# Kernel tuning notes

Hardware: AMD Instinct MI355X
Metric: run time of the kernel (lower is better)

The kernel has to match this reference:

```python
import jax, jax.numpy as jnp
import numpy as np

DIM = 768
HEADS = 12
HEAD_DIM = DIM // HEADS
NUM_CLASSES = 1000
SCALE = HEAD_DIM ** (-0.5)


def setup_inputs() -> dict:
    key = jax.random.key(0)
    ks = jax.random.split(key, 6)
    B, N = 4, 2048
    s = 0.02
    return {
        "x": jax.random.normal(ks[0], (B, N, DIM), dtype=jnp.float32),
        "w_qkv": jax.random.normal(ks[1], (DIM, 3 * DIM), dtype=jnp.float32) * s,
        "w_proj": jax.random.normal(ks[2], (DIM, DIM), dtype=jnp.float32) * s,
        "b_proj": jax.random.normal(ks[3], (DIM,), dtype=jnp.float32) * s,
        "w_head": jax.random.normal(ks[4], (DIM, NUM_CLASSES), dtype=jnp.float32) * s,
        "b_head": jax.random.normal(ks[5], (NUM_CLASSES,), dtype=jnp.float32) * s,
    }


def reference(x, w_qkv, w_proj, b_proj, w_head, b_head):
    B, N, C = x.shape
    qkv = (x @ w_qkv).reshape(B, N, 3, HEADS, HEAD_DIM)
    qkv = jnp.transpose(qkv, (2, 0, 3, 1, 4))  # [3, B, H, N, hd]
    q, k, v = qkv[0], qkv[1], qkv[2]
    attn = jnp.einsum("bhnd,bhmd->bhnm", q, k) * SCALE  # [B,H,N,N]
    attn = jax.nn.softmax(attn, axis=-1)
    out = jnp.einsum("bhnm,bhmd->bhnd", attn, v)  # [B,H,N,hd]
    out = jnp.transpose(out, (0, 2, 1, 3)).reshape(B, N, C)
    out = out @ w_proj + b_proj
    out = out @ w_head + b_head  # [B,N,num_classes]
    return jnp.max(out, axis=1)  # [B,num_classes]
```

## Files before the change

### kernel.cpp

```cpp
#include <hip/hip_runtime.h>
#include <hip/hip_bf16.h>

typedef __attribute__((ext_vector_type(8))) short short8;
typedef __attribute__((ext_vector_type(4))) float f32x4;
typedef __attribute__((ext_vector_type(16))) float f32x16;
typedef unsigned short u16t;
typedef unsigned int u32t;

#define MFMA16(a, b, c) __builtin_amdgcn_mfma_f32_16x16x32_bf16((a), (b), (c), 0, 0, 0)
#define MFMA32(a, b, c) __builtin_amdgcn_mfma_f32_32x32x16_bf16((a), (b), (c), 0, 0, 0)

__device__ __forceinline__ u16t f2b(float f) {
    union { float f; u32t u; } v; v.f = f;
    u32t u = v.u + 0x7FFFu + ((v.u >> 16) & 1u);
    return (u16t)(u >> 16);
}
__device__ __forceinline__ u32t encf(float f) {
    union { float f; u32t u; } v; v.f = f;
    return (v.u & 0x80000000u) ? ~v.u : (v.u | 0x80000000u);
}
__device__ __forceinline__ float decf(u32t u) {
    union { u32t u; float f; } v;
    v.u = (u & 0x80000000u) ? (u ^ 0x80000000u) : ~u;
    return v.f;
}
__device__ __forceinline__ float fexp2(float x) {
#if __has_builtin(__builtin_amdgcn_exp2f)
    return __builtin_amdgcn_exp2f(x);
#else
    return __expf(x * 0.6931471805599453f);
#endif
}
__device__ __forceinline__ void gload16(const u16t* g, u16t* l) {
    __builtin_amdgcn_global_load_lds((const __attribute__((address_space(1))) void*)g,
                                     (__attribute__((address_space(3))) void*)l, 16, 0, 0);
}

__global__ __launch_bounds__(256) void k_cast_x(const float* __restrict__ x, u16t* __restrict__ xb) {
    int i = blockIdx.x * 256 + threadIdx.x;
    float4 v = ((const float4*)x)[i];
    ushort4 o;
    o.x = f2b(v.x); o.y = f2b(v.y); o.z = f2b(v.z); o.w = f2b(v.w);
    ((ushort4*)xb)[i] = o;
}

__global__ __launch_bounds__(256) void k_transpose(const float* __restrict__ W, u16t* __restrict__ WT,
                                                   int K, int N, int NP) {
    __shared__ float t[32][33];
    int n0 = blockIdx.x * 32, k0 = blockIdx.y * 32;
    int tx = threadIdx.x, ty = threadIdx.y;
    for (int i = 0; i < 32; i += 8) {
        int k = k0 + ty + i, n = n0 + tx;
        t[ty + i][tx] = (n < N) ? W[(size_t)k * N + n] : 0.f;
    }
    __syncthreads();
    for (int i = 0; i < 32; i += 8) {
        int n = n0 + ty + i, k = k0 + tx;
        if (n < NP) WT[(size_t)n * K + k] = f2b(t[tx][ty + i]);
    }
}

__global__ __launch_bounds__(256) void k_bias_f(const float* __restrict__ bproj, const float* __restrict__ whead,
                                                const float* __restrict__ bhead, float* __restrict__ bf) {
    __shared__ float red[256];
    int t = threadIdx.x;
    int c = t & 15;
    int jg = t >> 4;
    int n = blockIdx.x * 16 + c;
    float s = 0.f;
    if (n < 1000) {
#pragma unroll 4
        for (int j = jg * 48; j < jg * 48 + 48; ++j)
            s += bproj[j] * whead[j * 1000 + n];
    }
    red[t] = s;
    __syncthreads();
    for (int off = 128; off >= 16; off >>= 1) {
        if (t < off) red[t] += red[t + off];
        __syncthreads();
    }
    if (t < 16) {
        int nn = blockIdx.x * 16 + t;
        bf[nn] = (nn < 1000) ? (red[t] + bhead[nn]) : 0.f;
    }
}

__global__ __launch_bounds__(256) void k_init_out(u32t* __restrict__ o, int n) {
    int i = blockIdx.x * 256 + threadIdx.x;
    if (i < n) o[i] = 0u;
}
__global__ __launch_bounds__(256) void k_decode_out(u32t* __restrict__ o, int n) {
    int i = blockIdx.x * 256 + threadIdx.x;
    if (i < n) {
        float f = decf(o[i]);
        ((float*)o)[i] = f;
    }
}

#define BM 256
#define BN 128

#define QSCALE 0.18033688011112042f

template <int EPI>
__global__ __launch_bounds__(512, 2) void k_gemm8(const u16t* __restrict__ A, const u16t* __restrict__ BT,
                                                  int M, int N, int K,
                                                  u16t* __restrict__ Cb, const float* __restrict__ bias,
                                                  u32t* __restrict__ omax) {
    __shared__ alignas(16) u16t Asf[2 * 2 * 8192];
    __shared__ alignas(16) u16t Bsf[2 * 2 * 4096];

    int tid = threadIdx.x;
    int lane = tid & 63, wid = tid >> 6;
    int wr = wid >> 1, wc = wid & 1;
    int g = lane >> 4, l15 = lane & 15;

    int nwg = gridDim.x;
    int bid = blockIdx.x;
    int wg = (bid & 7) * (nwg >> 3) + (bid >> 3);
    int nx = N >> 7;
    int bx = wg % nx, by = wg / nx;
    int m0 = by * BM, n0 = bx * BN;

    f32x4 acc[4][4];
    for (int i = 0; i < 4; i++)
        for (int j = 0; j < 4; j++) acc[i][j] = (f32x4){0.f, 0.f, 0.f, 0.f};

    const u16t* srcA[4]; u16t* dstA[4];
#pragma unroll
    for (int ii = 0; ii < 4; ii++) {
        int kk = ii >> 1;
        int cl = wid * 128 + (ii & 1) * 64 + lane;
        int cd = cl ^ ((cl >> 3) & 3);
        int arow = cd >> 2, acolc = cd & 3;
        srcA[ii] = A + (size_t)(m0 + arow) * K + kk * 32 + acolc * 8;
        dstA[ii] = &Asf[kk * 8192 + cl * 8];
    }
    const u16t* srcB[2]; u16t* dstB[2];
#pragma unroll
    for (int jj = 0; jj < 2; jj++) {
        int c = (wid * 2 + jj) * 64 + lane;
        int kk = c >> 9, cl = c & 511;
        int cd = cl ^ ((cl >> 3) & 3);
        srcB[jj] = BT + (size_t)(n0 + (cd >> 2)) * K + kk * 32 + (cd & 3) * 8;
        dstB[jj] = &Bsf[kk * 4096 + cl * 8];
    }

    int aoff[4], boff[4];
#pragma unroll
    for (int i = 0; i < 4; i++) {
        int lin = ((wr * 64 + i * 16 + l15) << 6) + (g << 4);
        aoff[i] = (lin ^ (((lin >> 7) & 3) << 4)) >> 1;
    }
#pragma unroll
    for (int j = 0; j < 4; j++) {
        int lin = ((wc * 64 + j * 16 + l15) << 6) + (g << 4);
        boff[j] = (lin ^ (((lin >> 7) & 3) << 4)) >> 1;
    }

#pragma unroll
    for (int ii = 0; ii < 4; ii++) gload16(srcA[ii], dstA[ii]);
#pragma unroll
    for (int jj = 0; jj < 2; jj++) gload16(srcB[jj], dstB[jj]);

    const int NT = K >> 6;

#pragma unroll 1
    for (int t = 0; t < NT; ++t) {
        const int d = t & 1, nd = d ^ 1;
        if (t + 1 < NT) {
            int ko = (t + 1) << 6;
            gload16(srcA[0] + ko, dstA[0] + nd * 16384);
            gload16(srcA[1] + ko, dstA[1] + nd * 16384);
            gload16(srcB[0] + ko, dstB[0] + nd * 8192);
            gload16(srcB[1] + ko, dstB[1] + nd * 8192);
            asm volatile("s_waitcnt vmcnt(4)" ::: "memory");
        } else {
            asm volatile("s_waitcnt vmcnt(0)" ::: "memory");
        }
        __builtin_amdgcn_s_barrier();

        const u16t* Ab = &Asf[d * 16384];
        const u16t* Bb = &Bsf[d * 8192];

        short8 af[4], bf[4];
#pragma unroll
        for (int i = 0; i < 4; i++) af[i] = *(const short8*)&Ab[aoff[i]];
#pragma unroll
        for (int j = 0; j < 4; j++) bf[j] = *(const short8*)&Bb[boff[j]];
        __builtin_amdgcn_s_setprio(1);
#pragma unroll
        for (int i = 0; i < 4; i++)
#pragma unroll
            for (int j = 0; j < 4; j++) acc[i][j] = MFMA16(af[i], bf[j], acc[i][j]);
        __builtin_amdgcn_s_setprio(0);

        if (t + 1 < NT) {
            int ko = (t + 1) << 6;
            gload16(srcA[2] + ko, dstA[2] + nd * 16384);
            gload16(srcA[3] + ko, dstA[3] + nd * 16384);
        }

#pragma unroll
        for (int i = 0; i < 4; i++) af[i] = *(const short8*)&Ab[8192 + aoff[i]];
#pragma unroll
        for (int j = 0; j < 4; j++) bf[j] = *(const short8*)&Bb[4096 + boff[j]];
        __builtin_amdgcn_s_setprio(1);
#pragma unroll
        for (int i = 0; i < 4; i++)
#pragma unroll
            for (int j = 0; j < 4; j++) acc[i][j] = MFMA16(af[i], bf[j], acc[i][j]);
        __builtin_amdgcn_s_setprio(0);

        asm volatile("s_waitcnt lgkmcnt(0)" ::: "memory");
        __builtin_amdgcn_s_barrier();
    }

    if constexpr (EPI == 0) {
        for (int i = 0; i < 4; i++)
            for (int j = 0; j < 4; j++)
                for (int r = 0; r < 4; r++) {
                    int row = m0 + wr * 64 + i * 16 + g * 4 + r;
                    int col = n0 + wc * 64 + j * 16 + l15;
                    int t = col / 768, rem = col - t * 768;
                    int hh = rem >> 6, d = rem & 63;
                    int bb = row >> 11, n = row & 2047;
                    float v = acc[i][j][r];
                    size_t idx;
                    if (t == 0) {
                        v *= QSCALE;
                        idx = ((size_t)(bb * 12 + hh)) * 131072 + (size_t)n * 64 + d;
                    } else if (t == 1) {
                        idx = ((size_t)(48 + bb * 12 + hh)) * 131072 + (size_t)n * 64 + d;
                    } else {
                        int np = (n & ~12) | ((n & 4) << 1) | ((n & 8) >> 1);
                        idx = ((size_t)(96 + bb * 12 + hh)) * 131072 + (size_t)d * 2048 + np;
                    }
                    Cb[idx] = f2b(v);
                }
    } else if constexpr (EPI == 3) {
        for (int i = 0; i < 4; i++)
            for (int j = 0; j < 4; j++)
                for (int r = 0; r < 4; r++) {
                    int row = m0 + wr * 64 + i * 16 + g * 4 + r;
                    int col = n0 + wc * 64 + j * 16 + l15;
                    Cb[(size_t)row * N + col] = f2b(acc[i][j][r]);
                }
    } else {
        __shared__ float smax[4][BN];
        float cmax[4];
        for (int j = 0; j < 4; j++) {
            float m = -3.0e38f;
            for (int i = 0; i < 4; i++)
                for (int r = 0; r < 4; r++) m = fmaxf(m, acc[i][j][r]);
            m = fmaxf(m, __shfl_xor(m, 16));
            m = fmaxf(m, __shfl_xor(m, 32));
            cmax[j] = m;
        }
        __syncthreads();
        if (lane < 16)
            for (int j = 0; j < 4; j++) smax[wr][wc * 64 + j * 16 + lane] = cmax[j];
        __syncthreads();
        if (tid < BN) {
            int col = n0 + tid;
            if (col < 1000) {
                float m = fmaxf(fmaxf(smax[0][tid], smax[1][tid]),
                                fmaxf(smax[2][tid], smax[3][tid])) + bias[col];
                int b = m0 >> 11;
                atomicMax(&omax[b * 1000 + col], encf(m));
            }
        }
    }
}

__global__ __launch_bounds__(256) void k_flash(const u16t* __restrict__ QKV, u16t* __restrict__ AO) {
    __shared__ alignas(16) u16t Kc[3][4096];
    __shared__ alignas(16) u16t Vc[3][4096];

    const int tid = threadIdx.x;
    const int lane = tid & 63;
    const int h = lane >> 5;
    const int l31 = lane & 31;
    const int w = tid >> 6;
    const int wk = ((blockIdx.x & 7) * 96) + (blockIdx.x >> 3);
    const int qt = wk & 15;
    const int hb = wk >> 4;
    const int head = hb % 12, b = hb / 12;
    const u16t* Qg = QKV + ((size_t)hb) * 131072;
    const u16t* Kg = QKV + ((size_t)(48 + hb)) * 131072;
    const u16t* Vg = QKV + ((size_t)(96 + hb)) * 131072;
    const int q0w = qt * 128 + w * 32;

    short8 qf[4];
#pragma unroll
    for (int ks = 0; ks < 4; ++ks)
        qf[ks] = *(const short8*)&Qg[(size_t)(q0w + l31) * 64 + ks * 16 + h * 8];
    asm volatile("s_waitcnt vmcnt(0)" ::: "memory");

    short8 vone;
#pragma unroll
    for (int e = 0; e < 8; ++e) vone[e] = (short)0x3F80;

    f32x16 o0, o1, lsum;
#pragma unroll
    for (int r = 0; r < 16; ++r) { o0[r] = 0.f; o1[r] = 0.f; lsum[r] = 0.f; }

    auto stage = [&](int bi, int kv0) {
#pragma unroll
        for (int c = 0; c < 2; ++c) {
            int ic = c * 256 + tid;
            int ss = ic >> 8, ks = (ic >> 6) & 3, l6 = ic & 63;
            int hh = l6 >> 5, lq = l6 & 31;
            const u16t* gs = Kg + ((size_t)(kv0 + ss * 32 + lq) << 6) + ks * 16 + hh * 8;
            gload16(gs, &Kc[bi][ic * 8]);
        }
#pragma unroll
        for (int c = 0; c < 2; ++c) {
            int ic = c * 256 + tid;
            int jb = ic >> 8, ks = (ic >> 6) & 3, l6 = ic & 63;
            int hh = l6 >> 5, ld = l6 & 31;
            const u16t* gs = Vg + (size_t)(jb * 32 + ld) * 2048 + kv0 + ks * 16 + hh * 8;
            gload16(gs, &Vc[bi][ic * 8]);
        }
    };

    stage(0, 0);
    stage(1, 64);

#pragma unroll 1
    for (int t = 0; t < 32; ++t) {
        const int cur = t % 3;
        if (t < 30) {
            stage((t + 2) % 3, (t + 2) * 64);
            asm volatile("s_waitcnt vmcnt(8)" ::: "memory");
        } else if (t == 30) {
            asm volatile("s_waitcnt vmcnt(4)" ::: "memory");
        } else {
            asm volatile("s_waitcnt vmcnt(0)" ::: "memory");
        }
        __builtin_amdgcn_s_barrier();

        const u16t* Kb = &Kc[cur][0];
        const u16t* Vb = &Vc[cur][0];

        f32x16 s0, s1;
#pragma unroll
        for (int r = 0; r < 16; ++r) { s0[r] = 0.f; s1[r] = 0.f; }
        __builtin_amdgcn_s_setprio(1);
#pragma unroll
        for (int ks = 0; ks < 4; ++ks) {
            short8 k0 = *(const short8*)&Kb[(ks * 64 + lane) * 8];
            short8 k1 = *(const short8*)&Kb[((4 + ks) * 64 + lane) * 8];
            s0 = MFMA32(k0, qf[ks], s0);
            s1 = MFMA32(k1, qf[ks], s1);
        }
        __builtin_amdgcn_s_setprio(0);

        short8 pf[4];
        auto packhalf = [&](const f32x16& sv, int half, int idx) {
            union { u32t wu[4]; short8 v; } u;
#pragma unroll
            for (int wq = 0; wq < 4; ++wq) {
                float lo = fexp2(sv[half * 8 + 2 * wq]);
                float hi = fexp2(sv[half * 8 + 2 * wq + 1]);
                asm("v_cvt_pk_bf16_f32 %0, %1, %2" : "=v"(u.wu[wq]) : "v"(lo), "v"(hi));
            }
            pf[idx] = u.v;
        };
        packhalf(s0, 0, 0);
        packhalf(s0, 1, 1);
        packhalf(s1, 0, 2);
        packhalf(s1, 1, 3);

        __builtin_amdgcn_s_setprio(1);
#pragma unroll
        for (int ks = 0; ks < 4; ++ks) {
            short8 v0 = *(const short8*)&Vb[(ks * 64 + lane) * 8];
            short8 v1 = *(const short8*)&Vb[((4 + ks) * 64 + lane) * 8];
            o0 = MFMA32(pf[ks], v0, o0);
            o1 = MFMA32(pf[ks], v1, o1);
            lsum = MFMA32(pf[ks], vone, lsum);
        }
        __builtin_amdgcn_s_setprio(0);

        asm volatile("s_waitcnt lgkmcnt(0)" ::: "memory");
        __builtin_amdgcn_s_barrier();
    }

#pragma unroll
    for (int r = 0; r < 16; ++r) {
        int q = (r & 3) + 8 * (r >> 2) + 4 * h;
        float rn = 1.0f / lsum[r];
        u16t* dst = AO + (size_t)(b * 2048 + q0w + q) * 768 + head * 64;
        dst[l31] = f2b(o0[r] * rn);
        dst[32 + l31] = f2b(o1[r] * rn);
    }
}

extern "C" void kernel_launch(void* const* d_in, const int* in_sizes, int n_in,
                              void* d_out, int out_size, void* d_ws, size_t ws_size,
                              hipStream_t stream) {
    const float* x = (const float*)d_in[0];
    const float* w_qkv = (const float*)d_in[1];
    const float* w_proj = (const float*)d_in[2];
    const float* b_proj = (const float*)d_in[3];
    const float* w_head = (const float*)d_in[4];
    const float* b_head = (const float*)d_in[5];

    char* ws = (char*)d_ws;
    u16t* xb = (u16t*)(ws);
    u16t* wqkvT = (u16t*)(ws + 12582912);
    u16t* wheadT = (u16t*)(ws + 16121856);
    u16t* wprojb = (u16t*)(ws + 17694720);
    u16t* qkv = (u16t*)(ws + 18874368);
    u16t* ao = (u16t*)(ws + 56623104);
    u16t* WfT = (u16t*)(ws + 69206016);
    float* bias_f = (float*)(ws + 70778880);

    dim3 tb(32, 8);
    k_cast_x<<<6144, 256, 0, stream>>>(x, xb);
    k_cast_x<<<576, 256, 0, stream>>>(w_proj, (u16t*)wprojb);
    k_transpose<<<dim3(2304 / 32, 768 / 32), tb, 0, stream>>>(w_qkv, wqkvT, 768, 2304, 2304);
    k_transpose<<<dim3(1024 / 32, 768 / 32), tb, 0, stream>>>(w_head, wheadT, 768, 1000, 1024);
    k_init_out<<<16, 256, 0, stream>>>((u32t*)d_out, 4000);
    k_bias_f<<<64, 256, 0, stream>>>(b_proj, w_head, b_head, bias_f);

    k_gemm8<3><<<24, 512, 0, stream>>>(wheadT, wprojb, 1024, 768, 768, WfT, nullptr, nullptr);

    k_gemm8<0><<<576, 512, 0, stream>>>(xb, wqkvT, 8192, 2304, 768, qkv, nullptr, nullptr);
    k_flash<<<768, 256, 0, stream>>>(qkv, ao);
    k_gemm8<2><<<256, 512, 0, stream>>>(ao, WfT, 8192, 1024, 768, nullptr, bias_f, (u32t*)d_out);

    k_decode_out<<<16, 256, 0, stream>>>((u32t*)d_out, 4000);
}
```

Before: 213.2 us.

## Triple-buffer GEMM shared memory and interleave loads with MFMA sub-phases

The GEMM kernel moves from a double-buffered to a triple-buffered LDS ring, prefetching two K-tiles ahead. Each iteration is split into four MFMA sub-phases separated by barriers, with global-to-LDS loads for the tile two steps ahead issued between them. The aim is to hide global memory latency more deeply and keep the matrix units busy. In exchange, LDS use rises to about 144KB per block, so occupancy drops to one block per CU (launch bounds changed to 512,1), and the extra barriers add synchronization cost.

```diff
diff --git a/kernel.cpp b/kernel.cpp
--- a/kernel.cpp
+++ b/kernel.cpp
@@ -103,12 +103,12 @@
 #define QSCALE 0.18033688011112042f
 
 template <int EPI>
-__global__ __launch_bounds__(512, 2) void k_gemm8(const u16t* __restrict__ A, const u16t* __restrict__ BT,
+__global__ __launch_bounds__(512, 1) void k_gemm9(const u16t* __restrict__ A, const u16t* __restrict__ BT,
                                                   int M, int N, int K,
                                                   u16t* __restrict__ Cb, const float* __restrict__ bias,
                                                   u32t* __restrict__ omax) {
-    __shared__ alignas(16) u16t Asf[2 * 2 * 8192];
-    __shared__ alignas(16) u16t Bsf[2 * 2 * 4096];
+    __shared__ alignas(16) u16t Asf[3][2][8192];
+    __shared__ alignas(16) u16t Bsf[3][2][4096];
 
     int tid = threadIdx.x;
     int lane = tid & 63, wid = tid >> 6;
@@ -126,24 +126,23 @@
     for (int i = 0; i < 4; i++)
         for (int j = 0; j < 4; j++) acc[i][j] = (f32x4){0.f, 0.f, 0.f, 0.f};
 
-    const u16t* srcA[4]; u16t* dstA[4];
+    const u16t* srcA[4]; int offA[4];
 #pragma unroll
     for (int ii = 0; ii < 4; ii++) {
         int kk = ii >> 1;
         int cl = wid * 128 + (ii & 1) * 64 + lane;
         int cd = cl ^ ((cl >> 3) & 3);
-        int arow = cd >> 2, acolc = cd & 3;
-        srcA[ii] = A + (size_t)(m0 + arow) * K + kk * 32 + acolc * 8;
-        dstA[ii] = &Asf[kk * 8192 + cl * 8];
-    }
-    const u16t* srcB[2]; u16t* dstB[2];
+        srcA[ii] = A + (size_t)(m0 + (cd >> 2)) * K + kk * 32 + (cd & 3) * 8;
+        offA[ii] = kk * 8192 + cl * 8;
+    }
+    const u16t* srcB[2]; int offB[2];
 #pragma unroll
     for (int jj = 0; jj < 2; jj++) {
         int c = (wid * 2 + jj) * 64 + lane;
         int kk = c >> 9, cl = c & 511;
         int cd = cl ^ ((cl >> 3) & 3);
         srcB[jj] = BT + (size_t)(n0 + (cd >> 2)) * K + kk * 32 + (cd & 3) * 8;
-        dstB[jj] = &Bsf[kk * 4096 + cl * 8];
+        offB[jj] = kk * 4096 + cl * 8;
     }
 
     int aoff[4], boff[4];
@@ -158,61 +157,92 @@
         boff[j] = (lin ^ (((lin >> 7) & 3) << 4)) >> 1;
     }
 
-#pragma unroll
-    for (int ii = 0; ii < 4; ii++) gload16(srcA[ii], dstA[ii]);
-#pragma unroll
-    for (int jj = 0; jj < 2; jj++) gload16(srcB[jj], dstB[jj]);
-
     const int NT = K >> 6;
+
+#pragma unroll
+    for (int ii = 0; ii < 4; ii++) gload16(srcA[ii], &Asf[0][0][0] + offA[ii]);
+#pragma unroll
+    for (int jj = 0; jj < 2; jj++) gload16(srcB[jj], &Bsf[0][0][0] + offB[jj]);
+#pragma unroll
+    for (int ii = 0; ii < 4; ii++) gload16(srcA[ii] + 64, &Asf[1][0][0] + offA[ii]);
+#pragma unroll
+    for (int jj = 0; jj < 2; jj++) gload16(srcB[jj] + 64, &Bsf[1][0][0] + offB[jj]);
 
 #pragma unroll 1
     for (int t = 0; t < NT; ++t) {
-        const int d = t & 1, nd = d ^ 1;
+        const int cb = t % 3;
+        const int sb = (t + 2) % 3;
+        const bool st = (t + 2) < NT;
+        const int ko = (t + 2) << 6;
+
         if (t + 1 < NT) {
-            int ko = (t + 1) << 6;
-            gload16(srcA[0] + ko, dstA[0] + nd * 16384);
-            gload16(srcA[1] + ko, dstA[1] + nd * 16384);
-            gload16(srcB[0] + ko, dstB[0] + nd * 8192);
-            gload16(srcB[1] + ko, dstB[1] + nd * 8192);
-            asm volatile("s_waitcnt vmcnt(4)" ::: "memory");
+            asm volatile("s_waitcnt vmcnt(6)" ::: "memory");
         } else {
             asm volatile("s_waitcnt vmcnt(0)" ::: "memory");
         }
         __builtin_amdgcn_s_barrier();
 
-        const u16t* Ab = &Asf[d * 16384];
-        const u16t* Bb = &Bsf[d * 8192];
-
-        short8 af[4], bf[4];
-#pragma unroll
-        for (int i = 0; i < 4; i++) af[i] = *(const short8*)&Ab[aoff[i]];
-#pragma unroll
-        for (int j = 0; j < 4; j++) bf[j] = *(const short8*)&Bb[boff[j]];
-        __builtin_amdgcn_s_setprio(1);
-#pragma unroll
-        for (int i = 0; i < 4; i++)
-#pragma unroll
-            for (int j = 0; j < 4; j++) acc[i][j] = MFMA16(af[i], bf[j], acc[i][j]);
-        __builtin_amdgcn_s_setprio(0);
-
-        if (t + 1 < NT) {
-            int ko = (t + 1) << 6;
-            gload16(srcA[2] + ko, dstA[2] + nd * 16384);
-            gload16(srcA[3] + ko, dstA[3] + nd * 16384);
-        }
-
-#pragma unroll
-        for (int i = 0; i < 4; i++) af[i] = *(const short8*)&Ab[8192 + aoff[i]];
-#pragma unroll
-        for (int j = 0; j < 4; j++) bf[j] = *(const short8*)&Bb[4096 + boff[j]];
-        __builtin_amdgcn_s_setprio(1);
-#pragma unroll
-        for (int i = 0; i < 4; i++)
-#pragma unroll
-            for (int j = 0; j < 4; j++) acc[i][j] = MFMA16(af[i], bf[j], acc[i][j]);
-        __builtin_amdgcn_s_setprio(0);
-
-        asm volatile("s_waitcnt lgkmcnt(0)" ::: "memory");
+        const u16t* Ab = &Asf[cb][0][0];
+        const u16t* Bb = &Bsf[cb][0][0];
+        u16t* Asb = &Asf[sb][0][0];
+        u16t* Bsb = &Bsf[sb][0][0];
+
+        short8 a0, a1, a2, a3, b0, b1, b2, b3;
+
+        if (st) { gload16(srcA[0] + ko, Asb + offA[0]); gload16(srcA[1] + ko, Asb + offA[1]); }
+        a0 = *(const short8*)&Ab[aoff[0]];
+        a1 = *(const short8*)&Ab[aoff[1]];
+        b0 = *(const short8*)&Bb[boff[0]];
+        b1 = *(const short8*)&Bb[boff[1]];
+        b2 = *(const short8*)&Bb[boff[2]];
+        b3 = *(const short8*)&Bb[boff[3]];
+        __builtin_amdgcn_s_barrier();
+        __builtin_amdgcn_s_setprio(1);
+        acc[0][0] = MFMA16(a0, b0, acc[0][0]); acc[0][1] = MFMA16(a0, b1, acc[0][1]);
+        acc[0][2] = MFMA16(a0, b2, acc[0][2]); acc[0][3] = MFMA16(a0, b3, acc[0][3]);
+        acc[1][0] = MFMA16(a1, b0, acc[1][0]); acc[1][1] = MFMA16(a1, b1, acc[1][1]);
+        acc[1][2] = MFMA16(a1, b2, acc[1][2]); acc[1][3] = MFMA16(a1, b3, acc[1][3]);
+        __builtin_amdgcn_s_setprio(0);
+        __builtin_amdgcn_s_barrier();
+
+        if (st) { gload16(srcA[2] + ko, Asb + offA[2]); gload16(srcA[3] + ko, Asb + offA[3]); }
+        a2 = *(const short8*)&Ab[aoff[2]];
+        a3 = *(const short8*)&Ab[aoff[3]];
+        __builtin_amdgcn_s_barrier();
+        __builtin_amdgcn_s_setprio(1);
+        acc[2][0] = MFMA16(a2, b0, acc[2][0]); acc[2][1] = MFMA16(a2, b1, acc[2][1]);
+        acc[2][2] = MFMA16(a2, b2, acc[2][2]); acc[2][3] = MFMA16(a2, b3, acc[2][3]);
+        acc[3][0] = MFMA16(a3, b0, acc[3][0]); acc[3][1] = MFMA16(a3, b1, acc[3][1]);
+        acc[3][2] = MFMA16(a3, b2, acc[3][2]); acc[3][3] = MFMA16(a3, b3, acc[3][3]);
+        __builtin_amdgcn_s_setprio(0);
+        __builtin_amdgcn_s_barrier();
+
+        if (st) { gload16(srcB[0] + ko, Bsb + offB[0]); }
+        a0 = *(const short8*)&Ab[8192 + aoff[0]];
+        a1 = *(const short8*)&Ab[8192 + aoff[1]];
+        b0 = *(const short8*)&Bb[4096 + boff[0]];
+        b1 = *(const short8*)&Bb[4096 + boff[1]];
+        b2 = *(const short8*)&Bb[4096 + boff[2]];
+        b3 = *(const short8*)&Bb[4096 + boff[3]];
+        __builtin_amdgcn_s_barrier();
+        __builtin_amdgcn_s_setprio(1);
+        acc[0][0] = MFMA16(a0, b0, acc[0][0]); acc[0][1] = MFMA16(a0, b1, acc[0][1]);
+        acc[0][2] = MFMA16(a0, b2, acc[0][2]); acc[0][3] = MFMA16(a0, b3, acc[0][3]);
+        acc[1][0] = MFMA16(a1, b0, acc[1][0]); acc[1][1] = MFMA16(a1, b1, acc[1][1]);
+        acc[1][2] = MFMA16(a1, b2, acc[1][2]); acc[1][3] = MFMA16(a1, b3, acc[1][3]);
+        __builtin_amdgcn_s_setprio(0);
+        __builtin_amdgcn_s_barrier();
+
+        if (st) { gload16(srcB[1] + ko, Bsb + offB[1]); }
+        a2 = *(const short8*)&Ab[8192 + aoff[2]];
+        a3 = *(const short8*)&Ab[8192 + aoff[3]];
+        __builtin_amdgcn_s_barrier();
+        __builtin_amdgcn_s_setprio(1);
+        acc[2][0] = MFMA16(a2, b0, acc[2][0]); acc[2][1] = MFMA16(a2, b1, acc[2][1]);
+        acc[2][2] = MFMA16(a2, b2, acc[2][2]); acc[2][3] = MFMA16(a2, b3, acc[2][3]);
+        acc[3][0] = MFMA16(a3, b0, acc[3][0]); acc[3][1] = MFMA16(a3, b1, acc[3][1]);
+        acc[3][2] = MFMA16(a3, b2, acc[3][2]); acc[3][3] = MFMA16(a3, b3, acc[3][3]);
+        __builtin_amdgcn_s_setprio(0);
         __builtin_amdgcn_s_barrier();
     }
 
@@ -425,11 +455,11 @@
     k_init_out<<<16, 256, 0, stream>>>((u32t*)d_out, 4000);
     k_bias_f<<<64, 256, 0, stream>>>(b_proj, w_head, b_head, bias_f);
 
-    k_gemm8<3><<<24, 512, 0, stream>>>(wheadT, wprojb, 1024, 768, 768, WfT, nullptr, nullptr);
-
-    k_gemm8<0><<<576, 512, 0, stream>>>(xb, wqkvT, 8192, 2304, 768, qkv, nullptr, nullptr);
+    k_gemm9<3><<<24, 512, 0, stream>>>(wheadT, wprojb, 1024, 768, 768, WfT, nullptr, nullptr);
+
+    k_gemm9<0><<<576, 512, 0, stream>>>(xb, wqkvT, 8192, 2304, 768, qkv, nullptr, nullptr);
     k_flash<<<768, 256, 0, stream>>>(qkv, ao);
-    k_gemm8<2><<<256, 512, 0, stream>>>(ao, WfT, 8192, 1024, 768, nullptr, bias_f, (u32t*)d_out);
+    k_gemm9<2><<<256, 512, 0, stream>>>(ao, WfT, 8192, 1024, 768, nullptr, bias_f, (u32t*)d_out);
 
     k_decode_out<<<16, 256, 0, stream>>>((u32t*)d_out, 4000);
 }
```

New measurement: 239.3 us. 1.12x slower.
